# Kernel tuning notes

Hardware: AMD Instinct MI355X
Metric: run time of the kernel (lower is better)

## Reference

```python
import jax, jax.numpy as jnp
import numpy as np

NEG = -100000.0
V, E, HID, K = 30000, 256, 512, 32   # vocab, embed_dim, hidden_size, tag_size
H = HID // 2                          # per-direction LSTM hidden
B, T = 128, 512                       # batch, seq_len
START, END = K - 2, K - 1


def setup_inputs() -> dict:
    keys = iter(jax.random.split(jax.random.key(0), 40))

    def u(shape, scale):
        return jax.random.uniform(next(keys), shape, jnp.float32, -scale, scale)

    inp = {}
    inp["words"] = jax.random.randint(next(keys), (B, T), 0, V)
    inp["labels"] = jax.random.randint(next(keys), (B, T), 0, K - 2)
    inp["emb"] = jax.random.normal(next(keys), (V, E), jnp.float32)
    s = 1.0 / float(np.sqrt(H))
    for l, din in [(0, E), (1, HID)]:
        for d in ("f", "b"):
            inp[f"Wih{l}{d}"] = u((4 * H, din), s)
            inp[f"Whh{l}{d}"] = u((4 * H, H), s)
            inp[f"b{l}{d}"] = u((4 * H,), s)
    st = 1.0 / float(np.sqrt(HID))
    inp["Wtag"] = u((K, HID), st)
    inp["btag"] = u((K,), st)
    tm = u((K, K), float(np.sqrt(3.0 / K)))  # kaiming-uniform-like
    inp["trans"] = tm.at[START, :].set(NEG).at[:, END].set(NEG)
    return inp


def _lstm_dir(x, Wih, Whh, b, reverse):
    # x: [T, B, Din] seq-major; standard torch LSTM cell, gate order i,f,g,o
    Hd = Whh.shape[1]
    z = jnp.zeros((x.shape[1], Hd), x.dtype)

    def step(carry, xt):
        h, c = carry
        g = xt @ Wih.T + h @ Whh.T + b
        i, f, gg, o = jnp.split(g, 4, axis=-1)
        c = jax.nn.sigmoid(f) * c + jax.nn.sigmoid(i) * jnp.tanh(gg)
        h = jax.nn.sigmoid(o) * jnp.tanh(c)
        return (h, c), h

    _, hs = jax.lax.scan(step, (z, z), x, reverse=reverse)
    return hs  # [T, B, Hd], aligned with x even when reverse=True


def reference(words, labels, emb, Wih0f, Whh0f, b0f, Wih0b, Whh0b, b0b,
              Wih1f, Whh1f, b1f, Wih1b, Whh1b, b1b, Wtag, btag, trans):
    x = emb[words].transpose(1, 0, 2)  # [T, B, E]
    h1 = jnp.concatenate([_lstm_dir(x, Wih0f, Whh0f, b0f, False),
                          _lstm_dir(x, Wih0b, Whh0b, b0b, True)], axis=-1)
    h2 = jnp.concatenate([_lstm_dir(h1, Wih1f, Whh1f, b1f, False),
                          _lstm_dir(h1, Wih1b, Whh1b, b1b, True)], axis=-1)
    emit = h2 @ Wtag.T + btag          # [T, B, K]
    lab = labels.T                     # [T, B]
    Bn = lab.shape[1]

    # ---- gold path score ----
    prev = jnp.concatenate([jnp.full((1, Bn), START, lab.dtype), lab], axis=0)
    cur = jnp.concatenate([lab, jnp.full((1, Bn), END, lab.dtype)], axis=0)
    gold_trans = trans[cur, prev].sum(axis=0)                                   # [B]
    gold_emit = jnp.take_along_axis(emit, lab[:, :, None], axis=-1)[..., 0].sum(axis=0)
    gold = gold_trans + gold_emit

    # ---- log partition (forward algorithm) ----
    dp0 = jnp.full((Bn, K), NEG, emit.dtype).at[:, START].set(0.0)

    def part_step(dp, e_t):
        cur_logit = trans[None] + e_t[:, :, None] + dp[:, None, :]  # [B, K_cur, K_prev]
        return jax.nn.logsumexp(cur_logit, axis=-1), None

    dp, _ = jax.lax.scan(part_step, dp0, emit)
    logZ = jax.nn.logsumexp(dp + trans[END][None, :], axis=-1)
    nll = jnp.mean(logZ - gold)

    # ---- viterbi (max-plus DP + backtrace) ----
    def vit_step(dp_v, e_t):
        cur_score = trans[None] + e_t[:, :, None] + dp_v[:, None, :]
        return cur_score.max(axis=-1), cur_score.argmax(axis=-1)

    dpv, bps = jax.lax.scan(vit_step, dp0, emit)   # bps: [T, B, K]
    dpv = dpv + trans[END][None, :]
    best = dpv.argmax(axis=-1)                      # [B]

    def back(tag, bp_t):
        prev_tag = jnp.take_along_axis(bp_t, tag[:, None], axis=1)[:, 0]
        return prev_tag, tag

    _, path = jax.lax.scan(back, best, bps, reverse=True)  # [T, B]
    return nll, path.T
```

## Files before the change

### kernel.cpp

```cpp
#include <hip/hip_runtime.h>
#include <math.h>

#define T_LEN 512
#define BATCH 128
#define KTAG  32
#define START_TAG 30
#define END_TAG   31
#define NEGV  -100000.0f

#define L2E    1.4426950408889634f
#define TWOL2E 2.8853900817779268f
#define LN2    0.6931471805599453f

typedef __attribute__((ext_vector_type(4))) short bf16x4;
typedef __attribute__((ext_vector_type(8))) short bf16x8;
typedef __attribute__((ext_vector_type(4))) float f32x4;
#define MFMA16   __builtin_amdgcn_mfma_f32_16x16x32_bf16
#define MFMA16F8 __builtin_amdgcn_mfma_f32_16x16x32_fp8_fp8
#define EXP2(x)  __builtin_amdgcn_exp2f(x)
#define RCP(x)   __builtin_amdgcn_rcpf(x)

__device__ __forceinline__ short f2bf(float x) {
    unsigned int u = __float_as_uint(x);
    u += 0x7fffu + ((u >> 16) & 1u);
    return (short)(u >> 16);
}

__device__ __forceinline__ f32x4 bf4_to_f32x4(bf16x4 v) {
    union { bf16x4 s; uint2 u; } c; c.s = v;
    f32x4 r;
    r[0] = __uint_as_float(c.u.x << 16);
    r[1] = __uint_as_float(c.u.x & 0xffff0000u);
    r[2] = __uint_as_float(c.u.y << 16);
    r[3] = __uint_as_float(c.u.y & 0xffff0000u);
    return r;
}

__device__ __forceinline__ unsigned char f2fp8(float x) {
    unsigned u = __float_as_uint(x);
    unsigned s = (u >> 24) & 0x80u;
    unsigned mag = u & 0x7fffffffu;
    if (mag >= 0x43e80000u) return (unsigned char)(s | 0x7e);
    int e = (int)(mag >> 23) - 127;
    int ulp_exp = (e < -6) ? -9 : (e - 3);
    float C = __uint_as_float((unsigned)((ulp_exp + 23 + 127) << 23)) * 1.5f;
    float r = (__uint_as_float(mag) + C) - C;
    unsigned ru = __float_as_uint(r);
    int re = (int)(ru >> 23) - 127;
    unsigned code;
    if (r == 0.0f) code = 0;
    else if (re < -6) code = (unsigned)(r * 512.0f);
    else code = (unsigned)((re + 7) << 3) | ((ru >> 20) & 7u);
    return (unsigned char)(s | code);
}

__device__ __forceinline__ unsigned pack2_fp8(float h0, float h1) {
#if __has_builtin(__builtin_amdgcn_cvt_pk_fp8_f32)
    return (unsigned)__builtin_amdgcn_cvt_pk_fp8_f32(h0, h1, 0, false);
#else
    return (unsigned)f2fp8(h0) | ((unsigned)f2fp8(h1) << 8);
#endif
}

__global__ void fill_kernel(float* out, int n, float v) {
    int i = blockIdx.x * 256 + threadIdx.x;
    if (i < n) out[i] = v;
}

__device__ __forceinline__ void dev_pack_bf16(const float* __restrict__ W,
                                              short* __restrict__ out, int K, int idx) {
    const int KT = K >> 5;
    int i  = idx & 7;
    int ln = (idx >> 3) & 63;
    int rem = idx >> 9;
    int kt = rem % KT;
    int wt = rem / KT;
    int type = wt & 3, w = wt >> 2;
    int row = type * 256 + w * 16 + (ln & 15);
    int col = kt * 32 + ((ln >> 4) << 3) + i;
    float sc = (type == 2) ? TWOL2E : L2E;
    out[idx] = f2bf(W[(size_t)row * K + col] * sc);
}

__device__ __forceinline__ void dev_pack_fp8(const float* __restrict__ W,
                                             unsigned char* __restrict__ out, int K, int idx) {
    const int KT = K >> 5;
    int i  = idx & 7;
    int ln = (idx >> 3) & 63;
    int rem = idx >> 9;
    int kt = rem % KT;
    int wt = rem / KT;
    int type = wt & 3, w = wt >> 2;
    int row = type * 256 + w * 16 + (ln & 15);
    int col = kt * 32 + ((ln >> 4) << 3) + i;
    float sc = (type == 2) ? TWOL2E : L2E;
    out[idx] = f2fp8(W[(size_t)row * K + col] * sc);
}

__device__ __forceinline__ void dev_pack_wtag(const float* __restrict__ Wtag,
                                              unsigned char* __restrict__ out, int idx) {
    int i  = idx & 7;
    int ln = (idx >> 3) & 63;
    int kt = (idx >> 9) & 7;
    int nt = (idx >> 12) & 1;
    int dir = idx >> 13;
    int row = nt * 16 + (ln & 15);
    int col = dir * 256 + kt * 32 + ((ln >> 4) << 3) + i;
    out[idx] = f2fp8(Wtag[row * 512 + col]);
}

__global__ __launch_bounds__(256) void pack_all(
    const float* Wih0f, const float* Wih0b, const float* Wih1f, const float* Wih1b,
    const float* Whh0f, const float* Whh0b, const float* Whh1f, const float* Whh1b,
    const float* Wtag, const float* emb,
    short* wq0f, short* wq0b, short* wq1f, short* wq1b,
    unsigned char* h80f, unsigned char* h80b, unsigned char* h81f, unsigned char* h81b,
    unsigned char* wtag8, short* embq)
{
    const int bx = blockIdx.x;
    const int tid = threadIdx.x;
    if (bx < 2048) {
        const float* W = (bx < 1024) ? Wih0f : Wih0b;
        short* o = (bx < 1024) ? wq0f : wq0b;
        dev_pack_bf16(W, o, 256, (bx & 1023) * 256 + tid);
    } else if (bx < 6144) {
        const float* W = (bx < 4096) ? Wih1f : Wih1b;
        short* o = (bx < 4096) ? wq1f : wq1b;
        dev_pack_bf16(W, o, 512, ((bx - 2048) & 2047) * 256 + tid);
    } else if (bx < 10240) {
        int seg = (bx - 6144) >> 10;
        const float* W = (seg == 0) ? Whh0f : (seg == 1) ? Whh0b : (seg == 2) ? Whh1f : Whh1b;
        unsigned char* o = (seg == 0) ? h80f : (seg == 1) ? h80b : (seg == 2) ? h81f : h81b;
        dev_pack_fp8(W, o, 256, ((bx - 6144) & 1023) * 256 + tid);
    } else if (bx < 10304) {
        dev_pack_wtag(Wtag, wtag8, (bx - 10240) * 256 + tid);
    } else {
        int i = (bx - 10304) * 256 + tid;
        embq[i] = f2bf(emb[i]);
    }
}

template <int LAYER, int AMODE>
__device__ __forceinline__ void gemm_role(
    int gb, int C, const int* __restrict__ words, const void* __restrict__ Asrc,
    const short* __restrict__ BfF, const short* __restrict__ BfB,
    const float* __restrict__ bsF, const float* __restrict__ bsB,
    short* __restrict__ preF, short* __restrict__ preB, int s0, char* smraw)
{
    constexpr int K  = (LAYER == 0) ? 256 : 512;
    constexpr int KT = K / 32;
    constexpr int RB = K * 2;
    constexpr int NT = (LAYER == 0) ? 2 : 1;
    constexpr int NH = 4 / NT;

    const int dir = gb / (NH * C);
    int rem = gb - dir * NH * C;
    const int half = rem / C;
    const int gx = rem - half * C;
    const int sblk = gx >> 3, bg = gx & 7;
    const int t0 = half * NT;
    const int tid = threadIdx.x;
    const int wv = tid >> 6, L = tid & 63;
    const int wid = wv;
    const int brow = L & 15, kgrp = L >> 4;

    const short* Bf = dir ? BfB : BfF;
    const float* bias = dir ? bsB : bsF;
    short* pre = dir ? preB : preF;
    short* As = (short*)smraw;

    const bf16x8* Bp = (const bf16x8*)Bf;
    bf16x8 bw[NT][KT];
#pragma unroll
    for (int u = 0; u < NT; ++u)
#pragma unroll
        for (int kt = 0; kt < KT; ++kt)
            bw[u][kt] = Bp[(((wid * 4 + t0 + u) * KT + kt) << 6) + L];

    float bb[NT];
#pragma unroll
    for (int u = 0; u < NT; ++u) {
        float sc = ((t0 + u) == 2) ? TWOL2E : L2E;
        bb[u] = bias[(t0 + u) * 256 + wid * 16 + brow] * sc;
    }

    for (int sl = 0; sl < 8; ++sl) {
        const int sloc = sblk * 8 + sl;
        const int t = dir ? (T_LEN - 1 - (s0 + sloc)) : (s0 + sloc);

        {
            char* lds = (char*)As;
            if (LAYER == 0) {
                if (tid < 512) {
                    const int row = tid >> 5, ch = tid & 31;
                    const int b = bg * 16 + row;
                    const int cb = ch * 16;
                    const int word = words[b * T_LEN + t];
                    if (AMODE == 0) {
                        const char* src = (const char*)Asrc + (size_t)word * 512 + cb;
                        *(bf16x8*)(lds + ((row * RB + cb) ^ ((row & 7) << 4))) = *(const bf16x8*)src;
                    } else {
                        const float* src = (const float*)Asrc + (size_t)word * 256 + ch * 8;
                        float4 f0 = *(const float4*)(src);
                        float4 f1 = *(const float4*)(src + 4);
                        short tmp[8] = {f2bf(f0.x), f2bf(f0.y), f2bf(f0.z), f2bf(f0.w),
                                        f2bf(f1.x), f2bf(f1.y), f2bf(f1.z), f2bf(f1.w)};
                        *(bf16x8*)(lds + ((row * RB + cb) ^ ((row & 7) << 4))) = *(const bf16x8*)tmp;
                    }
                }
            } else {
                const int row = tid >> 6, ch = tid & 63;
                const int b = bg * 16 + row;
                const int cb = ch * 16;
                const char* src = (const char*)Asrc + ((size_t)t * BATCH + b) * 1024 + cb;
                *(bf16x8*)(lds + ((row * RB + cb) ^ ((row & 7) << 4))) = *(const bf16x8*)src;
            }
        }
        __syncthreads();

        f32x4 acc[NT];
#pragma unroll
        for (int u = 0; u < NT; ++u) acc[u] = (f32x4){bb[u], bb[u], bb[u], bb[u]};

        const char* lds = (const char*)As;
#pragma unroll
        for (int kt = 0; kt < KT; ++kt) {
            bf16x8 a = *(const bf16x8*)(lds + ((brow * RB + kt * 64 + kgrp * 16) ^ ((brow & 7) << 4)));
#pragma unroll
            for (int u = 0; u < NT; ++u)
                acc[u] = MFMA16(a, bw[u][kt], acc[u], 0, 0, 0);
        }

        bf16x4* pp = (bf16x4*)pre;
        const size_t base = ((((size_t)sloc * 8 + bg) * 16 + wid) * 4 + t0) * 64 + L;
#pragma unroll
        for (int u = 0; u < NT; ++u) {
            bf16x4 o = {f2bf(acc[u][0]), f2bf(acc[u][1]), f2bf(acc[u][2]), f2bf(acc[u][3])};
            pp[base + (size_t)u * 64] = o;
        }
        __syncthreads();
    }
}

__global__ __launch_bounds__(1024) void gemm_only0(
    const int* words, const void* Asrc, const short* BfF, const short* BfB,
    const float* bsF, const float* bsB, short* preF, short* preB, int s0, int C, int amode)
{
    constexpr int SMB = 8192;
    __shared__ __align__(16) char smraw[SMB];
    if (amode == 0)
        gemm_role<0, 0>(blockIdx.x, C, words, Asrc, BfF, BfB, bsF, bsB, preF, preB, s0, smraw);
    else
        gemm_role<0, 1>(blockIdx.x, C, words, Asrc, BfF, BfB, bsF, bsB, preF, preB, s0, smraw);
}

__global__ __launch_bounds__(1024) void gemm_only1(
    const int* words, const void* Asrc, const short* BfF, const short* BfB,
    const float* bsF, const float* bsB, short* preF, short* preB, int s0, int C)
{
    constexpr int SMB = 16384;
    __shared__ __align__(16) char smraw[SMB];
    gemm_role<1, 2>(blockIdx.x, C, words, Asrc, BfF, BfB, bsF, bsB, preF, preB, s0, smraw);
}

template <int LAYER, int AMODE>
__global__ __launch_bounds__(1024) void fused_chunk(
    const int* __restrict__ words, const void* __restrict__ xsrc,
    const short* __restrict__ wihF, const short* __restrict__ wihB,
    const float* __restrict__ biasF, const float* __restrict__ biasB,
    short* __restrict__ preOutF, short* __restrict__ preOutB, int s0g, int gemm_on,
    const short* __restrict__ preF, const short* __restrict__ preB,
    const unsigned char* __restrict__ whhF, const unsigned char* __restrict__ whhB,
    short* __restrict__ h1out,
    const unsigned char* __restrict__ wtagf, const float* __restrict__ btag,
    float* __restrict__ emitF, float* __restrict__ emitB,
    float* __restrict__ stC, long* __restrict__ stH,
    int s0, int C)
{
    constexpr int SMB = (LAYER == 1) ? (8704 + 32768) : 8704;
    __shared__ __align__(16) char smraw[SMB];

    if (blockIdx.x >= 32) {
        if (gemm_on)
            gemm_role<LAYER, AMODE>(blockIdx.x - 32, C, words, xsrc, wihF, wihB,
                                    biasF, biasB, preOutF, preOutB, s0g, smraw);
        return;
    }

    const int dir  = blockIdx.x >> 4;
    const int bg   = (blockIdx.x >> 1) & 7;
    const int half = blockIdx.x & 1;
    const int tid = threadIdx.x;
    const int wid = tid >> 6;
    const int L   = tid & 63;
    const int brow = L & 15;
    const int kgrp = L >> 4;
    const int Lp = (L + half * 32) & 63;

    const bf16x4* pre = (const bf16x4*)(dir ? preB : preF);
    long* hb0 = (long*)smraw;
    long* hb1 = (long*)(smraw + 4352);
    float (*ep)[8][16][32] = (float(*)[8][16][32])(smraw + 8704);

    const long* Wp = (const long*)(dir ? whhB : whhF);
    long whh[32];
#pragma unroll
    for (int tt = 0; tt < 4; ++tt)
#pragma unroll
        for (int kt = 0; kt < 8; ++kt)
            whh[tt * 8 + kt] = Wp[(((wid * 4 + tt) * 8 + kt) << 6) + L];

    long wt0 = 0, wt1 = 0;
    if (LAYER == 1) {
        int kw = (wid < 8) ? wid : 7;
        const long* wtp = (const long*)wtagf;
        wt0 = wtp[(((dir * 2 + 0) * 8 + kw) << 6) + L];
        wt1 = wtp[(((dir * 2 + 1) * 8 + kw) << 6) + L];
    }

    float cs0, cs1;
    if (s0 == 0) {
        for (int q = tid; q < 544; q += 1024) hb0[q] = 0;
        cs0 = cs1 = 0.f;
    } else {
        for (int q = tid; q < 544; q += 1024)
            hb0[q] = stH[(size_t)blockIdx.x * 544 + q];
        float2 c2 = ((const float2*)stC)[blockIdx.x * 1024 + tid];
        cs0 = c2.x; cs1 = c2.y;
    }
    for (int q = tid; q < 544; q += 1024) hb1[q] = 0;
    __syncthreads();

    const size_t pstride = 8 * 16 * 4 * 64;
    const size_t pbase = (((size_t)bg * 16 + wid) * 4) * 64 + Lp;
    bf16x4 pc0 = pre[pbase + 0 * 64];
    bf16x4 pc1 = pre[pbase + 1 * 64];
    bf16x4 pc2 = pre[pbase + 2 * 64];
    bf16x4 pc3 = pre[pbase + 3 * 64];

    const int srcL = L & 31;
    const bool lo = (L < 32);
    const int rb = ((srcL >> 4) << 2) + (lo ? 0 : 2);
    const int jj = wid * 16 + (L & 15);

    for (int s = s0; s < s0 + C; ++s) {
        const int sloc = s - s0;
        const int par = s & 1;
        const char* ldsr = (const char*)(par ? hb1 : hb0);
        char* ldsw = (char*)(par ? hb0 : hb1);

        f32x4 acc0 = bf4_to_f32x4(pc0);
        f32x4 acc1 = bf4_to_f32x4(pc1);
        f32x4 acc2 = bf4_to_f32x4(pc2);
        f32x4 acc3 = bf4_to_f32x4(pc3);

        {
            const int sl2 = (sloc + 1 < C) ? sloc + 1 : sloc;
            const size_t pb = (size_t)sl2 * pstride + pbase;
            pc0 = pre[pb + 0 * 64];
            pc1 = pre[pb + 1 * 64];
            pc2 = pre[pb + 2 * 64];
            pc3 = pre[pb + 3 * 64];
        }

#pragma unroll
        for (int kt = 0; kt < 8; ++kt) {
            long a = *(const long*)(ldsr + brow * 272 + kt * 32 + kgrp * 8);
            acc0 = MFMA16F8(a, whh[0 * 8 + kt], acc0, 0, 0, 0);
            acc1 = MFMA16F8(a, whh[1 * 8 + kt], acc1, 0, 0, 0);
            acc2 = MFMA16F8(a, whh[2 * 8 + kt], acc2, 0, 0, 0);
            acc3 = MFMA16F8(a, whh[3 * 8 + kt], acc3, 0, 0, 0);
        }

        if (LAYER == 1 && sloc >= 1 && wid < 8) {
            long a = *(const long*)(ldsr + brow * 272 + wid * 32 + kgrp * 8);
            f32x4 e0 = {0.f, 0.f, 0.f, 0.f}, e1 = {0.f, 0.f, 0.f, 0.f};
            e0 = MFMA16F8(a, wt0, e0, 0, 0, 0);
            e1 = MFMA16F8(a, wt1, e1, 0, 0, 0);
#pragma unroll
            for (int r = 0; r < 4; ++r) {
                int bl = (kgrp << 2) + r;
                ep[par][wid][bl][brow] = e0[r];
                ep[par][wid][bl][16 + brow] = e1[r];
            }
        }

        if (LAYER == 1 && sloc >= 2 && tid < 256) {
            int bl = tid >> 5, tg = tid & 31;
            float v = 0.f;
#pragma unroll
            for (int p = 0; p < 8; ++p) v += ep[par ^ 1][p][bl][tg];
            const int x = s - 2;
            const int tp = dir ? (T_LEN - 1 - x) : x;
            size_t ei = ((size_t)tp * BATCH + bg * 16 + half * 8 + bl) * KTAG + tg;
            if (dir == 0) emitF[ei] = v + btag[tg];
            else          emitB[ei] = v;
        }

        float g0v0, g0v1, g1v0, g1v1, g2v0, g2v1, g3v0, g3v1;
        {
            float a00 = __shfl(acc0[2], srcL), a01 = __shfl(acc0[3], srcL);
            float a10 = __shfl(acc1[2], srcL), a11 = __shfl(acc1[3], srcL);
            float a20 = __shfl(acc2[2], srcL), a21 = __shfl(acc2[3], srcL);
            float a30 = __shfl(acc3[2], srcL), a31 = __shfl(acc3[3], srcL);
            g0v0 = lo ? acc0[0] : a00;  g0v1 = lo ? acc0[1] : a01;
            g1v0 = lo ? acc1[0] : a10;  g1v1 = lo ? acc1[1] : a11;
            g2v0 = lo ? acc2[0] : a20;  g2v1 = lo ? acc2[1] : a21;
            g3v0 = lo ? acc3[0] : a30;  g3v1 = lo ? acc3[1] : a31;
        }

        float hh0, hh1;
        {
            float ig, fg, gg, og;
            ig = RCP(1.0f + EXP2(-g0v0)); fg = RCP(1.0f + EXP2(-g1v0));
            gg = 1.0f - 2.0f * RCP(1.0f + EXP2(g2v0));
            og = RCP(1.0f + EXP2(-g3v0));
            cs0 = fg * cs0 + ig * gg;
            hh0 = og * (1.0f - 2.0f * RCP(1.0f + EXP2(TWOL2E * cs0)));
            ig = RCP(1.0f + EXP2(-g0v1)); fg = RCP(1.0f + EXP2(-g1v1));
            gg = 1.0f - 2.0f * RCP(1.0f + EXP2(g2v1));
            og = RCP(1.0f + EXP2(-g3v1));
            cs1 = fg * cs1 + ig * gg;
            hh1 = og * (1.0f - 2.0f * RCP(1.0f + EXP2(TWOL2E * cs1)));
        }

        {
            unsigned pk = pack2_fp8(hh0, hh1);
            ldsw[(rb + 0) * 272 + jj] = (char)(pk);
            ldsw[(rb + 1) * 272 + jj] = (char)(pk >> 8);
            if (LAYER == 0) {
                const int t = dir ? (T_LEN - 1 - s) : s;
                size_t gb = ((size_t)t * BATCH + bg * 16 + half * 8 + rb) * 512 + dir * 256 + jj;
                h1out[gb]       = f2bf(hh0);
                h1out[gb + 512] = f2bf(hh1);
            }
        }
        __syncthreads();
    }

    if (LAYER == 1) {
        if (wid < 8) {
            const char* ldsr = (const char*)hb0;
            long a = *(const long*)(ldsr + brow * 272 + wid * 32 + kgrp * 8);
            f32x4 e0 = {0.f, 0.f, 0.f, 0.f}, e1 = {0.f, 0.f, 0.f, 0.f};
            e0 = MFMA16F8(a, wt0, e0, 0, 0, 0);
            e1 = MFMA16F8(a, wt1, e1, 0, 0, 0);
#pragma unroll
            for (int r = 0; r < 4; ++r) {
                int bl = (kgrp << 2) + r;
                ep[0][wid][bl][brow] = e0[r];
                ep[0][wid][bl][16 + brow] = e1[r];
            }
        }
        if (tid < 256) {
            int bl = tid >> 5, tg = tid & 31;
            float v = 0.f;
#pragma unroll
            for (int p = 0; p < 8; ++p) v += ep[1][p][bl][tg];
            const int x = s0 + C - 2;
            const int tp = dir ? (T_LEN - 1 - x) : x;
            size_t ei = ((size_t)tp * BATCH + bg * 16 + half * 8 + bl) * KTAG + tg;
            if (dir == 0) emitF[ei] = v + btag[tg];
            else          emitB[ei] = v;
        }
        __syncthreads();
        if (tid < 256) {
            int bl = tid >> 5, tg = tid & 31;
            float v = 0.f;
#pragma unroll
            for (int p = 0; p < 8; ++p) v += ep[0][p][bl][tg];
            const int x = s0 + C - 1;
            const int tp = dir ? (T_LEN - 1 - x) : x;
            size_t ei = ((size_t)tp * BATCH + bg * 16 + half * 8 + bl) * KTAG + tg;
            if (dir == 0) emitF[ei] = v + btag[tg];
            else          emitB[ei] = v;
        }
    }

    for (int q = tid; q < 544; q += 1024)
        stH[(size_t)blockIdx.x * 544 + q] = hb0[q];
    ((float2*)stC)[blockIdx.x * 1024 + tid] = (float2){cs0, cs1};
}

__global__ __launch_bounds__(64) void crf_kernel(
    const float* __restrict__ emitF, const float* __restrict__ emitB,
    const float* __restrict__ trans, const int* __restrict__ labels,
    float* __restrict__ diff, float* __restrict__ path_out)
{
    const int lane = threadIdx.x;
    const int k = lane & 31;
    const int h = lane >> 5;
    const int p0 = h << 4;

    __shared__ unsigned char bps[T_LEN][KTAG];
    __shared__ unsigned char pth[T_LEN];

    const int bb = (blockIdx.x < BATCH) ? blockIdx.x : blockIdx.x - BATCH;
    float trow[16];
#pragma unroll
    for (int i = 0; i < 4; ++i) {
        float4 f = *(const float4*)(trans + k * KTAG + p0 + i * 4);
        trow[i * 4 + 0] = f.x; trow[i * 4 + 1] = f.y;
        trow[i * 4 + 2] = f.z; trow[i * 4 + 3] = f.w;
    }
    const float tend = trans[END_TAG * KTAG + k];

    size_t eidx = (size_t)bb * KTAG + k;

    if (blockIdx.x < BATCH) {
        const int b = bb;
        float trow2[16];
#pragma unroll
        for (int i = 0; i < 16; ++i) trow2[i] = trow[i] * L2E;
        float dp = (k == START_TAG) ? 0.0f : NEGV * L2E;
        float e2 = (emitF[eidx] + emitB[eidx]) * L2E;

        for (int t = 0; t < T_LEN; ++t) {
            float e_next2 = 0.0f;
            if (t + 1 < T_LEN) {
                size_t ei = ((size_t)(t + 1) * BATCH + b) * KTAG + k;
                e_next2 = (emitF[ei] + emitB[ei]) * L2E;
            }
            float v[16];
#pragma unroll
            for (int q = 0; q < 16; ++q)
                v[q] = trow2[q] + __shfl(dp, p0 + q);

            float mx[8];
#pragma unroll
            for (int i = 0; i < 8; ++i) mx[i] = fmaxf(v[i], v[i + 8]);
#pragma unroll
            for (int i = 0; i < 4; ++i) mx[i] = fmaxf(mx[i], mx[i + 4]);
            float halfm = fmaxf(fmaxf(mx[0], mx[1]), fmaxf(mx[2], mx[3]));
            float m = fmaxf(halfm, __shfl_xor(halfm, 32));

            float es[16];
#pragma unroll
            for (int i = 0; i < 16; ++i) es[i] = EXP2(v[i] - m);
#pragma unroll
            for (int i = 0; i < 8; ++i) es[i] += es[i + 8];
#pragma unroll
            for (int i = 0; i < 4; ++i) es[i] += es[i + 4];
            float shalf = (es[0] + es[1]) + (es[2] + es[3]);
            float ssum = shalf + __shfl_xor(shalf, 32);

            dp = e2 + m + __log2f(ssum);
            e2 = e_next2;
        }

        float fv = dp + tend * L2E;
        float mm = fv;
        for (int off = 16; off; off >>= 1) mm = fmaxf(mm, __shfl_xor(mm, off));
        float contrib = (lane < KTAG) ? EXP2(fv - mm) : 0.0f;
        float ss = contrib;
        for (int off = 32; off; off >>= 1) ss += __shfl_xor(ss, off);
        float logZ = (mm + __log2f(ss)) * LN2;

        float gsum = 0.0f;
        for (int t = lane; t < T_LEN; t += 64) {
            int curl = labels[b * T_LEN + t];
            int prev = (t > 0) ? labels[b * T_LEN + t - 1] : START_TAG;
            size_t gi = ((size_t)t * BATCH + b) * KTAG + curl;
            gsum += trans[curl * KTAG + prev] + emitF[gi] + emitB[gi];
        }
        if (lane == 0) gsum += trans[END_TAG * KTAG + labels[b * T_LEN + T_LEN - 1]];
        for (int off = 32; off; off >>= 1) gsum += __shfl_xor(gsum, off);

        if (lane == 0) diff[b] = logZ - gsum;
    } else {
        const int b = bb;
        float dpv = (k == START_TAG) ? 0.0f : NEGV;
        float e = emitF[eidx] + emitB[eidx];

        for (int t = 0; t < T_LEN; ++t) {
            float e_next = 0.0f;
            if (t + 1 < T_LEN) {
                size_t ei = ((size_t)(t + 1) * BATCH + b) * KTAG + k;
                e_next = emitF[ei] + emitB[ei];
            }
            float w[16];
#pragma unroll
            for (int q = 0; q < 16; ++q)
                w[q] = trow[q] + __shfl(dpv, p0 + q);

            float bv_[8]; int bi_[8];
#pragma unroll
            for (int i = 0; i < 8; ++i) {
                bool g = w[2 * i + 1] > w[2 * i];
                bv_[i] = g ? w[2 * i + 1] : w[2 * i];
                bi_[i] = p0 + (g ? 2 * i + 1 : 2 * i);
            }
#pragma unroll
            for (int i = 0; i < 4; ++i) {
                bool g = bv_[2 * i + 1] > bv_[2 * i];
                bv_[i] = g ? bv_[2 * i + 1] : bv_[2 * i];
                bi_[i] = g ? bi_[2 * i + 1] : bi_[2 * i];
            }
            {
                bool g = bv_[3] > bv_[2];
                bv_[1] = g ? bv_[3] : bv_[2];
                bi_[1] = g ? bi_[3] : bi_[2];
            }
            {
                bool g0 = bv_[1] > bv_[0];
                bv_[0] = g0 ? bv_[1] : bv_[0];
                bi_[0] = g0 ? bi_[1] : bi_[0];
            }
            float ov = __shfl_xor(bv_[0], 32);
            int   oi = __shfl_xor(bi_[0], 32);
            bool g2 = h ? (ov >= bv_[0]) : (ov > bv_[0]);
            float bm  = g2 ? ov : bv_[0];
            int  barg = g2 ? oi : bi_[0];

            dpv = e + bm;
            if (!h) bps[t][k] = (unsigned char)barg;
            e = e_next;
        }

        float bv = dpv + tend; int bi = k;
        for (int off = 16; off; off >>= 1) {
            float ovv = __shfl_xor(bv, off);
            int   oii = __shfl_xor(bi, off);
            if (ovv > bv || (ovv == bv && oii < bi)) { bv = ovv; bi = oii; }
        }

        __syncthreads();
        if (lane == 0) {
            int tag = bi;
            pth[T_LEN - 1] = (unsigned char)tag;
            for (int t = T_LEN - 2; t >= 0; --t) {
                tag = bps[t + 1][tag];
                pth[t] = (unsigned char)tag;
            }
        }
        __syncthreads();
        for (int t = lane; t < T_LEN; t += 64)
            path_out[(size_t)b * T_LEN + t] = (float)pth[t];
    }
}

__global__ void nll_kernel(const float* __restrict__ diff, float* __restrict__ out) {
    int lane = threadIdx.x;
    float v = diff[lane];
    __shared__ float red[2];
    for (int off = 32; off; off >>= 1) v += __shfl_xor(v, off);
    if ((lane & 63) == 0) red[lane >> 6] = v;
    __syncthreads();
    if (lane == 0) out[0] = (red[0] + red[1]) / 128.0f;
}

extern "C" void kernel_launch(void* const* d_in, const int* in_sizes, int n_in,
                              void* d_out, int out_size, void* d_ws, size_t ws_size,
                              hipStream_t stream) {
    (void)in_sizes; (void)n_in;

    const int*   words  = (const int*)d_in[0];
    const int*   labels = (const int*)d_in[1];
    const float* emb    = (const float*)d_in[2];
    const float* Wih0f  = (const float*)d_in[3];
    const float* Whh0f  = (const float*)d_in[4];
    const float* b0f    = (const float*)d_in[5];
    const float* Wih0b  = (const float*)d_in[6];
    const float* Whh0b  = (const float*)d_in[7];
    const float* b0b    = (const float*)d_in[8];
    const float* Wih1f  = (const float*)d_in[9];
    const float* Whh1f  = (const float*)d_in[10];
    const float* b1f    = (const float*)d_in[11];
    const float* Wih1b  = (const float*)d_in[12];
    const float* Whh1b  = (const float*)d_in[13];
    const float* b1b    = (const float*)d_in[14];
    const float* Wtag   = (const float*)d_in[15];
    const float* btag   = (const float*)d_in[16];
    const float* trans  = (const float*)d_in[17];
    float* out = (float*)d_out;
    char* ws = (char*)d_ws;

    const size_t WIH0B = (size_t)1024 * 256 * 2;
    const size_t WIH1B = (size_t)1024 * 512 * 2;
    const size_t WHH8B = (size_t)1024 * 256;
    const size_t WTAG8 = (size_t)16384;
    const size_t H1B   = (size_t)T_LEN * BATCH * 512 * 2;
    const size_t EMITB = (size_t)T_LEN * BATCH * KTAG * 4;
    const size_t EMBQB = (size_t)30000 * 256 * 2;
    const size_t STHB  = (size_t)32 * 544 * 8;
    const size_t STCB  = (size_t)32 * 1024 * 8;
    const size_t PSTEP = (size_t)BATCH * 1024 * 2;

    const size_t base0 = 2 * WIH0B + 2 * WIH1B + 4 * WHH8B + WTAG8 + H1B +
                         2 * EMITB + STHB + STCB + 4096 + (1u << 20);

    int C = 0, use_embq = 0;
    for (int eq = 1; eq >= 0 && !C; --eq)
        for (int c = 256; c >= 16 && !C; c >>= 1)
            if (base0 + (eq ? EMBQB : 0) + 4 * (size_t)c * PSTEP <= ws_size) {
                C = c; use_embq = eq;
            }
    if (!C) {
        fill_kernel<<<(out_size + 255) / 256, 256, 0, stream>>>(
            out, out_size, (float)(ws_size >> 20));
        return;
    }

    size_t off = 0;
    auto alloc = [&](size_t bytes) -> char* {
        char* p = ws + off;
        off = (off + bytes + 255) & ~(size_t)255;
        return p;
    };
    short* wihq0f = (short*)alloc(WIH0B);
    short* wihq0b = (short*)alloc(WIH0B);
    short* wihq1f = (short*)alloc(WIH1B);
    short* wihq1b = (short*)alloc(WIH1B);
    unsigned char* whh8_0f = (unsigned char*)alloc(WHH8B);
    unsigned char* whh8_0b = (unsigned char*)alloc(WHH8B);
    unsigned char* whh8_1f = (unsigned char*)alloc(WHH8B);
    unsigned char* whh8_1b = (unsigned char*)alloc(WHH8B);
    unsigned char* wtag8   = (unsigned char*)alloc(WTAG8);
    short* h1     = (short*)alloc(H1B);
    float* emF    = (float*)alloc(EMITB);
    float* emB    = (float*)alloc(EMITB);
    long*  stH    = (long*)alloc(STHB);
    float* stC    = (float*)alloc(STCB);
    float* diff   = (float*)alloc(4096);
    short* preFb[2], * preBb[2];
    preFb[0] = (short*)alloc((size_t)C * PSTEP);
    preFb[1] = (short*)alloc((size_t)C * PSTEP);
    preBb[0] = (short*)alloc((size_t)C * PSTEP);
    preBb[1] = (short*)alloc((size_t)C * PSTEP);
    short* embq = use_embq ? (short*)alloc(EMBQB) : nullptr;

    {
        int nblk = 10304 + (use_embq ? 30000 : 0);
        pack_all<<<nblk, 256, 0, stream>>>(
            Wih0f, Wih0b, Wih1f, Wih1b, Whh0f, Whh0b, Whh1f, Whh1b, Wtag, emb,
            wihq0f, wihq0b, wihq1f, wihq1b,
            whh8_0f, whh8_0b, whh8_1f, whh8_1b, wtag8, embq);
    }

    const int NC = T_LEN / C;
    const void* xsrc0 = use_embq ? (const void*)embq : (const void*)emb;
    const int am = use_embq ? 0 : 1;

    gemm_only0<<<4 * C, 1024, 0, stream>>>(words, xsrc0, wihq0f, wihq0b,
                                           b0f, b0b, preFb[0], preBb[0], 0, C, am);
    for (int c = 0; c < NC; ++c) {
        int on = (c + 1 < NC);
        if (use_embq)
            fused_chunk<0, 0><<<32 + 4 * C, 1024, 0, stream>>>(
                words, xsrc0, wihq0f, wihq0b, b0f, b0b,
                preFb[(c + 1) & 1], preBb[(c + 1) & 1], (c + 1) * C, on,
                preFb[c & 1], preBb[c & 1], whh8_0f, whh8_0b, h1,
                wtag8, btag, emF, emB, stC, stH, c * C, C);
        else
            fused_chunk<0, 1><<<32 + 4 * C, 1024, 0, stream>>>(
                words, xsrc0, wihq0f, wihq0b, b0f, b0b,
                preFb[(c + 1) & 1], preBb[(c + 1) & 1], (c + 1) * C, on,
                preFb[c & 1], preBb[c & 1], whh8_0f, whh8_0b, h1,
                wtag8, btag, emF, emB, stC, stH, c * C, C);
    }
    gemm_only1<<<8 * C, 1024, 0, stream>>>(nullptr, h1, wihq1f, wihq1b,
                                           b1f, b1b, preFb[0], preBb[0], 0, C);
    for (int c = 0; c < NC; ++c) {
        int on = (c + 1 < NC);
        fused_chunk<1, 2><<<32 + 8 * C, 1024, 0, stream>>>(
            nullptr, h1, wihq1f, wihq1b, b1f, b1b,
            preFb[(c + 1) & 1], preBb[(c + 1) & 1], (c + 1) * C, on,
            preFb[c & 1], preBb[c & 1], whh8_1f, whh8_1b, nullptr,
            wtag8, btag, emF, emB, stC, stH, c * C, C);
    }

    crf_kernel<<<256, 64, 0, stream>>>(emF, emB, trans, labels, diff, out + 1);
    nll_kernel<<<1, 128, 0, stream>>>(diff, out);
}
```

Baseline: 1.864 ms.

## Split CRF forward and Viterbi recurrences into meet-in-the-middle halves

```diff
diff --git a/kernel.cpp b/kernel.cpp
--- a/kernel.cpp
+++ b/kernel.cpp
@@ -482,42 +482,37 @@
     ((float2*)stC)[blockIdx.x * 1024 + tid] = (float2){cs0, cs1};
 }
 
-__global__ __launch_bounds__(64) void crf_kernel(
+__global__ __launch_bounds__(64) void crf_half(
     const float* __restrict__ emitF, const float* __restrict__ emitB,
-    const float* __restrict__ trans, const int* __restrict__ labels,
-    float* __restrict__ diff, float* __restrict__ path_out)
+    const float* __restrict__ trans,
+    float* __restrict__ alph, float* __restrict__ betap,
+    float* __restrict__ alphV, float* __restrict__ betaV,
+    unsigned char* __restrict__ bpsW, unsigned char* __restrict__ npsW)
 {
     const int lane = threadIdx.x;
     const int k = lane & 31;
     const int h = lane >> 5;
     const int p0 = h << 4;
-
-    __shared__ unsigned char bps[T_LEN][KTAG];
-    __shared__ unsigned char pth[T_LEN];
-
-    const int bb = (blockIdx.x < BATCH) ? blockIdx.x : blockIdx.x - BATCH;
-    float trow[16];
-#pragma unroll
-    for (int i = 0; i < 4; ++i) {
-        float4 f = *(const float4*)(trans + k * KTAG + p0 + i * 4);
-        trow[i * 4 + 0] = f.x; trow[i * 4 + 1] = f.y;
-        trow[i * 4 + 2] = f.z; trow[i * 4 + 3] = f.w;
-    }
-    const float tend = trans[END_TAG * KTAG + k];
-
-    size_t eidx = (size_t)bb * KTAG + k;
-
-    if (blockIdx.x < BATCH) {
-        const int b = bb;
+    const int role = blockIdx.x >> 7;
+    const int b = blockIdx.x & 127;
+
+    __shared__ unsigned char ptr_l[256 * KTAG];
+
+    if (role == 0) {
         float trow2[16];
 #pragma unroll
-        for (int i = 0; i < 16; ++i) trow2[i] = trow[i] * L2E;
+        for (int i = 0; i < 4; ++i) {
+            float4 f = *(const float4*)(trans + k * KTAG + p0 + i * 4);
+            trow2[i * 4 + 0] = f.x * L2E; trow2[i * 4 + 1] = f.y * L2E;
+            trow2[i * 4 + 2] = f.z * L2E; trow2[i * 4 + 3] = f.w * L2E;
+        }
         float dp = (k == START_TAG) ? 0.0f : NEGV * L2E;
-        float e2 = (emitF[eidx] + emitB[eidx]) * L2E;
-
-        for (int t = 0; t < T_LEN; ++t) {
+        size_t e0i = (size_t)b * KTAG + k;
+        float e2 = (emitF[e0i] + emitB[e0i]) * L2E;
+
+        for (int t = 0; t < 256; ++t) {
             float e_next2 = 0.0f;
-            if (t + 1 < T_LEN) {
+            if (t + 1 < 256) {
                 size_t ei = ((size_t)(t + 1) * BATCH + b) * KTAG + k;
                 e_next2 = (emitF[ei] + emitB[ei]) * L2E;
             }
@@ -525,7 +520,6 @@
 #pragma unroll
             for (int q = 0; q < 16; ++q)
                 v[q] = trow2[q] + __shfl(dp, p0 + q);
-
             float mx[8];
 #pragma unroll
             for (int i = 0; i < 8; ++i) mx[i] = fmaxf(v[i], v[i + 8]);
@@ -533,7 +527,6 @@
             for (int i = 0; i < 4; ++i) mx[i] = fmaxf(mx[i], mx[i + 4]);
             float halfm = fmaxf(fmaxf(mx[0], mx[1]), fmaxf(mx[2], mx[3]));
             float m = fmaxf(halfm, __shfl_xor(halfm, 32));
-
             float es[16];
 #pragma unroll
             for (int i = 0; i < 16; ++i) es[i] = EXP2(v[i] - m);
@@ -543,38 +536,66 @@
             for (int i = 0; i < 4; ++i) es[i] += es[i + 4];
             float shalf = (es[0] + es[1]) + (es[2] + es[3]);
             float ssum = shalf + __shfl_xor(shalf, 32);
-
             dp = e2 + m + __log2f(ssum);
             e2 = e_next2;
         }
-
-        float fv = dp + tend * L2E;
-        float mm = fv;
-        for (int off = 16; off; off >>= 1) mm = fmaxf(mm, __shfl_xor(mm, off));
-        float contrib = (lane < KTAG) ? EXP2(fv - mm) : 0.0f;
-        float ss = contrib;
-        for (int off = 32; off; off >>= 1) ss += __shfl_xor(ss, off);
-        float logZ = (mm + __log2f(ss)) * LN2;
-
-        float gsum = 0.0f;
-        for (int t = lane; t < T_LEN; t += 64) {
-            int curl = labels[b * T_LEN + t];
-            int prev = (t > 0) ? labels[b * T_LEN + t - 1] : START_TAG;
-            size_t gi = ((size_t)t * BATCH + b) * KTAG + curl;
-            gsum += trans[curl * KTAG + prev] + emitF[gi] + emitB[gi];
-        }
-        if (lane == 0) gsum += trans[END_TAG * KTAG + labels[b * T_LEN + T_LEN - 1]];
-        for (int off = 32; off; off >>= 1) gsum += __shfl_xor(gsum, off);
-
-        if (lane == 0) diff[b] = logZ - gsum;
-    } else {
-        const int b = bb;
+        if (lane < 32) alph[b * KTAG + k] = dp;
+    } else if (role == 1) {
+        float trowT2[16];
+#pragma unroll
+        for (int i = 0; i < 16; ++i)
+            trowT2[i] = trans[(p0 + i) * KTAG + k] * L2E;
+        float beta = trans[END_TAG * KTAG + k] * L2E;
+        size_t e0i = ((size_t)511 * BATCH + b) * KTAG + k;
+        float e2 = (emitF[e0i] + emitB[e0i]) * L2E;
+
+        for (int it = 0; it < 256; ++it) {
+            const int t = 510 - it;
+            float e_next2 = 0.0f;
+            if (it + 1 < 256) {
+                size_t ei = ((size_t)t * BATCH + b) * KTAG + k;
+                e_next2 = (emitF[ei] + emitB[ei]) * L2E;
+            }
+            float z = beta + e2;
+            float v[16];
+#pragma unroll
+            for (int q = 0; q < 16; ++q)
+                v[q] = trowT2[q] + __shfl(z, p0 + q);
+            float mx[8];
+#pragma unroll
+            for (int i = 0; i < 8; ++i) mx[i] = fmaxf(v[i], v[i + 8]);
+#pragma unroll
+            for (int i = 0; i < 4; ++i) mx[i] = fmaxf(mx[i], mx[i + 4]);
+            float halfm = fmaxf(fmaxf(mx[0], mx[1]), fmaxf(mx[2], mx[3]));
+            float m = fmaxf(halfm, __shfl_xor(halfm, 32));
+            float es[16];
+#pragma unroll
+            for (int i = 0; i < 16; ++i) es[i] = EXP2(v[i] - m);
+#pragma unroll
+            for (int i = 0; i < 8; ++i) es[i] += es[i + 8];
+#pragma unroll
+            for (int i = 0; i < 4; ++i) es[i] += es[i + 4];
+            float shalf = (es[0] + es[1]) + (es[2] + es[3]);
+            float ssum = shalf + __shfl_xor(shalf, 32);
+            beta = m + __log2f(ssum);
+            e2 = e_next2;
+        }
+        if (lane < 32) betap[b * KTAG + k] = beta;
+    } else if (role == 2) {
+        float trow[16];
+#pragma unroll
+        for (int i = 0; i < 4; ++i) {
+            float4 f = *(const float4*)(trans + k * KTAG + p0 + i * 4);
+            trow[i * 4 + 0] = f.x; trow[i * 4 + 1] = f.y;
+            trow[i * 4 + 2] = f.z; trow[i * 4 + 3] = f.w;
+        }
         float dpv = (k == START_TAG) ? 0.0f : NEGV;
-        float e = emitF[eidx] + emitB[eidx];
-
-        for (int t = 0; t < T_LEN; ++t) {
+        size_t e0i = (size_t)b * KTAG + k;
+        float e = emitF[e0i] + emitB[e0i];
+
+        for (int t = 0; t < 256; ++t) {
             float e_next = 0.0f;
-            if (t + 1 < T_LEN) {
+            if (t + 1 < 256) {
                 size_t ei = ((size_t)(t + 1) * BATCH + b) * KTAG + k;
                 e_next = emitF[ei] + emitB[ei];
             }
@@ -582,7 +603,6 @@
 #pragma unroll
             for (int q = 0; q < 16; ++q)
                 w[q] = trow[q] + __shfl(dpv, p0 + q);
-
             float bv_[8]; int bi_[8];
 #pragma unroll
             for (int i = 0; i < 8; ++i) {
@@ -596,47 +616,135 @@
                 bv_[i] = g ? bv_[2 * i + 1] : bv_[2 * i];
                 bi_[i] = g ? bi_[2 * i + 1] : bi_[2 * i];
             }
-            {
-                bool g = bv_[3] > bv_[2];
-                bv_[1] = g ? bv_[3] : bv_[2];
-                bi_[1] = g ? bi_[3] : bi_[2];
-            }
-            {
-                bool g0 = bv_[1] > bv_[0];
-                bv_[0] = g0 ? bv_[1] : bv_[0];
-                bi_[0] = g0 ? bi_[1] : bi_[0];
-            }
+            { bool g = bv_[3] > bv_[2]; bv_[1] = g ? bv_[3] : bv_[2]; bi_[1] = g ? bi_[3] : bi_[2]; }
+            { bool g = bv_[1] > bv_[0]; bv_[0] = g ? bv_[1] : bv_[0]; bi_[0] = g ? bi_[1] : bi_[0]; }
             float ov = __shfl_xor(bv_[0], 32);
             int   oi = __shfl_xor(bi_[0], 32);
             bool g2 = h ? (ov >= bv_[0]) : (ov > bv_[0]);
             float bm  = g2 ? ov : bv_[0];
             int  barg = g2 ? oi : bi_[0];
-
             dpv = e + bm;
-            if (!h) bps[t][k] = (unsigned char)barg;
+            if (!h) ptr_l[t * KTAG + k] = (unsigned char)barg;
             e = e_next;
         }
-
-        float bv = dpv + tend; int bi = k;
-        for (int off = 16; off; off >>= 1) {
-            float ovv = __shfl_xor(bv, off);
-            int   oii = __shfl_xor(bi, off);
-            if (ovv > bv || (ovv == bv && oii < bi)) { bv = ovv; bi = oii; }
-        }
-
-        __syncthreads();
-        if (lane == 0) {
-            int tag = bi;
-            pth[T_LEN - 1] = (unsigned char)tag;
-            for (int t = T_LEN - 2; t >= 0; --t) {
-                tag = bps[t + 1][tag];
-                pth[t] = (unsigned char)tag;
-            }
-        }
-        __syncthreads();
-        for (int t = lane; t < T_LEN; t += 64)
-            path_out[(size_t)b * T_LEN + t] = (float)pth[t];
-    }
+        if (lane < 32) alphV[b * KTAG + k] = dpv;
+        for (int i = lane; i < 2048; i += 64)
+            ((unsigned*)bpsW)[(size_t)b * 2048 + i] = ((const unsigned*)ptr_l)[i];
+    } else {
+        float trowT[16];
+#pragma unroll
+        for (int i = 0; i < 16; ++i)
+            trowT[i] = trans[(p0 + i) * KTAG + k];
+        float bvv = trans[END_TAG * KTAG + k];
+        size_t e0i = ((size_t)511 * BATCH + b) * KTAG + k;
+        float e = emitF[e0i] + emitB[e0i];
+
+        for (int it = 0; it < 256; ++it) {
+            const int t = 510 - it;
+            float e_next = 0.0f;
+            if (it + 1 < 256) {
+                size_t ei = ((size_t)t * BATCH + b) * KTAG + k;
+                e_next = emitF[ei] + emitB[ei];
+            }
+            float z = bvv + e;
+            float w[16];
+#pragma unroll
+            for (int q = 0; q < 16; ++q)
+                w[q] = trowT[q] + __shfl(z, p0 + q);
+            float bv_[8]; int bi_[8];
+#pragma unroll
+            for (int i = 0; i < 8; ++i) {
+                bool g = w[2 * i + 1] > w[2 * i];
+                bv_[i] = g ? w[2 * i + 1] : w[2 * i];
+                bi_[i] = p0 + (g ? 2 * i + 1 : 2 * i);
+            }
+#pragma unroll
+            for (int i = 0; i < 4; ++i) {
+                bool g = bv_[2 * i + 1] > bv_[2 * i];
+                bv_[i] = g ? bv_[2 * i + 1] : bv_[2 * i];
+                bi_[i] = g ? bi_[2 * i + 1] : bi_[2 * i];
+            }
+            { bool g = bv_[3] > bv_[2]; bv_[1] = g ? bv_[3] : bv_[2]; bi_[1] = g ? bi_[3] : bi_[2]; }
+            { bool g = bv_[1] > bv_[0]; bv_[0] = g ? bv_[1] : bv_[0]; bi_[0] = g ? bi_[1] : bi_[0]; }
+            float ov = __shfl_xor(bv_[0], 32);
+            int   oi = __shfl_xor(bi_[0], 32);
+            bool g2 = h ? (ov >= bv_[0]) : (ov > bv_[0]);
+            float bm  = g2 ? ov : bv_[0];
+            int  barg = g2 ? oi : bi_[0];
+            bvv = bm;
+            if (!h) ptr_l[(t - 255) * KTAG + k] = (unsigned char)barg;
+            e = e_next;
+        }
+        if (lane < 32) betaV[b * KTAG + k] = bvv;
+        for (int i = lane; i < 2048; i += 64)
+            ((unsigned*)npsW)[(size_t)b * 2048 + i] = ((const unsigned*)ptr_l)[i];
+    }
+}
+
+__global__ __launch_bounds__(64) void crf_join(
+    const float* __restrict__ emitF, const float* __restrict__ emitB,
+    const float* __restrict__ trans, const int* __restrict__ labels,
+    const float* __restrict__ alph, const float* __restrict__ betap,
+    const float* __restrict__ alphV, const float* __restrict__ betaV,
+    const unsigned char* __restrict__ bpsW, const unsigned char* __restrict__ npsW,
+    float* __restrict__ diff, float* __restrict__ path_out)
+{
+    const int b = blockIdx.x;
+    const int lane = threadIdx.x;
+    const int k = lane & 31;
+
+    __shared__ unsigned char bps_l[256 * KTAG];
+    __shared__ unsigned char nps_l[256 * KTAG];
+    __shared__ unsigned char pth[T_LEN];
+
+    for (int i = lane; i < 2048; i += 64) {
+        ((unsigned*)bps_l)[i] = ((const unsigned*)bpsW)[(size_t)b * 2048 + i];
+        ((unsigned*)nps_l)[i] = ((const unsigned*)npsW)[(size_t)b * 2048 + i];
+    }
+
+    float fv = alph[b * KTAG + k] + betap[b * KTAG + k];
+    float mm = fv;
+    for (int off = 16; off; off >>= 1) mm = fmaxf(mm, __shfl_xor(mm, off));
+    float contrib = (lane < KTAG) ? EXP2(fv - mm) : 0.0f;
+    float ss = contrib;
+    for (int off = 32; off; off >>= 1) ss += __shfl_xor(ss, off);
+    float logZ = (mm + __log2f(ss)) * LN2;
+
+    float gsum = 0.0f;
+    for (int t = lane; t < T_LEN; t += 64) {
+        int curl = labels[b * T_LEN + t];
+        int prev = (t > 0) ? labels[b * T_LEN + t - 1] : START_TAG;
+        size_t gi = ((size_t)t * BATCH + b) * KTAG + curl;
+        gsum += trans[curl * KTAG + prev] + emitF[gi] + emitB[gi];
+    }
+    if (lane == 0) gsum += trans[END_TAG * KTAG + labels[b * T_LEN + T_LEN - 1]];
+    for (int off = 32; off; off >>= 1) gsum += __shfl_xor(gsum, off);
+
+    float av = alphV[b * KTAG + k] + betaV[b * KTAG + k];
+    int bi = k;
+    for (int off = 16; off; off >>= 1) {
+        float ovv = __shfl_xor(av, off);
+        int   oii = __shfl_xor(bi, off);
+        if (ovv > av || (ovv == av && oii < bi)) { av = ovv; bi = oii; }
+    }
+
+    __syncthreads();
+    if (lane == 0) {
+        diff[b] = logZ - gsum;
+        int pb = bi, pf = bi;
+        pth[255] = (unsigned char)bi;
+        for (int i = 1; i <= 256; ++i) {
+            if (i <= 255) {
+                pb = bps_l[(256 - i) * KTAG + pb];
+                pth[255 - i] = (unsigned char)pb;
+            }
+            pf = nps_l[(i - 1) * KTAG + pf];
+            pth[255 + i] = (unsigned char)pf;
+        }
+    }
+    __syncthreads();
+    for (int t = lane; t < T_LEN; t += 64)
+        path_out[(size_t)b * T_LEN + t] = (float)pth[t];
 }
 
 __global__ void nll_kernel(const float* __restrict__ diff, float* __restrict__ out) {
@@ -685,9 +793,12 @@
     const size_t STHB  = (size_t)32 * 544 * 8;
     const size_t STCB  = (size_t)32 * 1024 * 8;
     const size_t PSTEP = (size_t)BATCH * 1024 * 2;
+    const size_t CRFAB = (size_t)4 * 128 * 32 * 4;
+    const size_t BPSB  = (size_t)128 * 256 * 32;
 
     const size_t base0 = 2 * WIH0B + 2 * WIH1B + 4 * WHH8B + WTAG8 + H1B +
-                         2 * EMITB + STHB + STCB + 4096 + (1u << 20);
+                         2 * EMITB + STHB + STCB + CRFAB + 2 * BPSB +
+                         4096 + (1u << 20);
 
     int C = 0, use_embq = 0;
     for (int eq = 1; eq >= 0 && !C; --eq)
@@ -722,12 +833,20 @@
     long*  stH    = (long*)alloc(STHB);
     float* stC    = (float*)alloc(STCB);
     float* diff   = (float*)alloc(4096);
+    float* crfa   = (float*)alloc(CRFAB);
+    unsigned char* bpsW = (unsigned char*)alloc(BPSB);
+    unsigned char* npsW = (unsigned char*)alloc(BPSB);
     short* preFb[2], * preBb[2];
     preFb[0] = (short*)alloc((size_t)C * PSTEP);
     preFb[1] = (short*)alloc((size_t)C * PSTEP);
     preBb[0] = (short*)alloc((size_t)C * PSTEP);
     preBb[1] = (short*)alloc((size_t)C * PSTEP);
     short* embq = use_embq ? (short*)alloc(EMBQB) : nullptr;
+
+    float* alph  = crfa;
+    float* betap = crfa + 128 * 32;
+    float* alphV = crfa + 2 * 128 * 32;
+    float* betaV = crfa + 3 * 128 * 32;
 
     {
         int nblk = 10304 + (use_embq ? 30000 : 0);
@@ -769,6 +888,10 @@
             wtag8, btag, emF, emB, stC, stH, c * C, C);
     }
 
-    crf_kernel<<<256, 64, 0, stream>>>(emF, emB, trans, labels, diff, out + 1);
+    crf_half<<<512, 64, 0, stream>>>(emF, emB, trans,
+                                     alph, betap, alphV, betaV, bpsW, npsW);
+    crf_join<<<128, 64, 0, stream>>>(emF, emB, trans, labels,
+                                     alph, betap, alphV, betaV, bpsW, npsW,
+                                     diff, out + 1);
     nll_kernel<<<1, 128, 0, stream>>>(diff, out);
 }
```

Measured after the change: 1.758 ms. -5.7%, faster.
